# Kernel optimization log

Hardware: AMD Instinct MI355X
Metric: run time of the kernel (lower is better)

Reference implementation:

```python
import jax, jax.numpy as jnp
import numpy as np

ALPHA = 0.2  # leaky relu slope
DEPTH = 3
MAX_REF = 10
MAX_DIR = 32

def leaky(x):
    return jnp.where(x >= 0, x, ALPHA * x)

def setup_inputs() -> dict:
    key = jax.random.key(0)
    ks = jax.random.split(key, 9)
    N, F_IN, F_OUT = 100000, 128, 128
    h = jax.random.normal(ks[0], (N, F_IN), dtype=jnp.float32)
    W_ref = jax.random.normal(ks[1], (F_IN, F_OUT), dtype=jnp.float32) * 0.1
    a_ref = jax.random.normal(ks[2], (2 * F_OUT, 1), dtype=jnp.float32) * 0.1
    W_dir = jax.random.normal(ks[3], (F_IN, F_OUT), dtype=jnp.float32) * 0.1
    a_dir = jax.random.normal(ks[4], (2 * F_OUT, 1), dtype=jnp.float32) * 0.1
    ref_neighbors = jax.random.randint(ks[5], (N, DEPTH + 1, MAX_REF), 0, N)
    ref_counts = jax.random.randint(ks[6], (N, DEPTH + 1), 0, MAX_REF + 1)
    dir_neighbors = jax.random.randint(ks[7], (N, MAX_DIR), 0, N)
    dir_counts = jax.random.randint(ks[8], (N,), 1, MAX_DIR + 1)
    return {"h": h, "W_ref": W_ref, "a_ref": a_ref, "W_dir": W_dir, "a_dir": a_dir,
            "ref_neighbors": ref_neighbors, "ref_counts": ref_counts,
            "dir_neighbors": dir_neighbors, "dir_counts": dir_counts}

def _forward_ref(h, W_ref, a_ref, ref_neighbors, ref_counts):
    Wh = h @ W_ref                                  # [N, F]
    F_ = Wh.shape[1]
    # mean of (up to 10) neighbor features per (node, depth); empty -> zeros
    nbr = Wh[ref_neighbors]                         # [N, D+1, 10, F]
    slot = jnp.arange(MAX_REF)[None, None, :]
    valid = slot < ref_counts[:, :, None]           # [N, D+1, 10]
    cnt = jnp.maximum(ref_counts, 1).astype(Wh.dtype)  # avoid div by 0
    f_ref = jnp.einsum('ndkf,ndk->ndf', nbr, valid.astype(Wh.dtype)) / cnt[:, :, None]  # [N, D+1, F]
    # attention score: leaky(cat(Wh[node], f_ref[d]) @ a_ref)
    a_self, a_nbr = a_ref[:F_, 0], a_ref[F_:, 0]
    e = leaky(Wh @ a_self[:, None] + f_ref @ a_nbr)  # [N,1]+[N,D+1] -> [N, D+1]
    alpha = jax.nn.softmax(e, axis=-1)
    out = jnp.einsum('ndf,nd->nf', f_ref, alpha)
    return jax.nn.sigmoid(out)

def _forward_dir(h, W_dir, a_dir, dir_neighbors, dir_counts):
    Wh = h @ W_dir                                  # [N, F]
    F_ = Wh.shape[1]
    nbr = Wh[dir_neighbors]                         # [N, K, F]
    a_self, a_nbr = a_dir[:F_, 0], a_dir[F_:, 0]
    e = leaky((Wh @ a_self)[:, None] + nbr @ a_nbr)  # [N, K]
    valid = jnp.arange(MAX_DIR)[None, :] < dir_counts[:, None]
    e = jnp.where(valid, e, -jnp.inf)
    alpha = jax.nn.softmax(e, axis=-1)
    out = jnp.einsum('nkf,nk->nf', nbr, alpha)
    return jax.nn.sigmoid(out)

def reference(h, W_ref, a_ref, W_dir, a_dir, ref_neighbors, ref_counts, dir_neighbors, dir_counts):
    h_ref = _forward_ref(h, W_ref, a_ref, ref_neighbors, ref_counts)
    h_dir = _forward_dir(h, W_dir, a_dir, dir_neighbors, dir_counts)
    return (h_ref + h_dir) / 2  # mode='mean'
```

## Files before the change

### kernel.cpp

```cpp
#include <hip/hip_runtime.h>

typedef __attribute__((ext_vector_type(8))) short s16x8;
typedef __attribute__((ext_vector_type(4))) float f32x4;
typedef __attribute__((ext_vector_type(2))) float f32x2;

#define F 128

__device__ __forceinline__ unsigned short f2bf(float f) {
    unsigned int u = __float_as_uint(f);
    u = (u + 0x7fffu + ((u >> 16) & 1u)) >> 16;
    return (unsigned short)u;
}
__device__ __forceinline__ float bflo(unsigned int u) { return __uint_as_float(u << 16); }
__device__ __forceinline__ float bfhi(unsigned int u) { return __uint_as_float(u & 0xffff0000u); }
__device__ __forceinline__ float leaky(float x) { return x >= 0.f ? x : 0.2f * x; }
__device__ __forceinline__ float sigmoidf(float x) { return 1.f / (1.f + __expf(-x)); }

#define SWZ16(row, b) ((b) ^ (((row) & 7) << 4))

__device__ __forceinline__ void glds16(void* lds, const void* g) {
    __builtin_amdgcn_global_load_lds(
        (const __attribute__((address_space(1))) unsigned int*)g,
        (__attribute__((address_space(3))) unsigned int*)lds,
        16, 0, 0);
}

__global__ __launch_bounds__(256) void prep_w(const float* __restrict__ wRef,
                                              const float* __restrict__ wDir,
                                              unsigned short* __restrict__ wT) {
    int i = blockIdx.x * 256 + threadIdx.x;
    int m = i >> 14;
    int rr = i & 16383;
    int k = rr >> 7;
    int c = rr & 127;
    const float* W = m ? wDir : wRef;
    wT[m * 16384 + c * 128 + (k ^ (((c & 7) << 3)))] = f2bf(W[k * 128 + c]);
}

__device__ __forceinline__ void epi(const f32x4* acc, unsigned char* cb ,
                                    int rowBase, int w, int r, int g, int lane, int N,
                                    const float* __restrict__ aVec,
                                    unsigned char* __restrict__ wh ,
                                    float* __restrict__ sArr, float* __restrict__ tArr) {
    float ps[4] = {0.f, 0.f, 0.f, 0.f}, pt[4] = {0.f, 0.f, 0.f, 0.f};
#pragma unroll
    for (int ct = 0; ct < 8; ++ct) {
        int c = ct * 16 + r;
        float As = aVec[c], At = aVec[128 + c];
#pragma unroll
        for (int q = 0; q < 4; ++q) { ps[q] += acc[ct][q] * As; pt[q] += acc[ct][q] * At; }
    }
#pragma unroll
    for (int off = 1; off <= 8; off <<= 1) {
#pragma unroll
        for (int q = 0; q < 4; ++q) {
            ps[q] += __shfl_xor(ps[q], off);
            pt[q] += __shfl_xor(pt[q], off);
        }
    }
    if (r == 0) {
#pragma unroll
        for (int q = 0; q < 4; ++q) {
            int row = rowBase + w * 16 + g * 4 + q;
            if (row < N) { sArr[row] = ps[q]; tArr[row] = pt[q]; }
        }
    }
#pragma unroll
    for (int ct = 0; ct < 8; ++ct) {
#pragma unroll
        for (int q = 0; q < 4; ++q) {
            int lrow = g * 4 + q;
            int xb = (ct * 16 + r) * 2;
            *(unsigned short*)(cb + lrow * 256 + SWZ16(lrow, xb)) = f2bf(acc[ct][q]);
        }
    }
#pragma unroll
    for (int i = 0; i < 4; ++i) {
        int off = i * 1024 + lane * 16;
        int lrow = off >> 8, x = off & 255;
        uint4 v = *(const uint4*)(cb + lrow * 256 + SWZ16(lrow, x));
        int pk0 = __builtin_amdgcn_cvt_pk_fp8_f32(bflo(v.x), bfhi(v.x), 0, false);
        pk0 = __builtin_amdgcn_cvt_pk_fp8_f32(bflo(v.y), bfhi(v.y), pk0, true);
        int pk1 = __builtin_amdgcn_cvt_pk_fp8_f32(bflo(v.z), bfhi(v.z), 0, false);
        pk1 = __builtin_amdgcn_cvt_pk_fp8_f32(bflo(v.w), bfhi(v.w), pk1, true);
        int grow = rowBase + w * 16 + lrow;
        if (grow < N) *(uint2*)(wh + (size_t)grow * 128 + (x >> 1)) = make_uint2((unsigned)pk0, (unsigned)pk1);
    }
}

__global__ __launch_bounds__(256) void gemm_wh(const float* __restrict__ h,
                                               const unsigned short* __restrict__ wT,
                                               const float* __restrict__ aRefG,
                                               const float* __restrict__ aDirG,
                                               unsigned char* __restrict__ whRef,
                                               unsigned char* __restrict__ whDir,
                                               float* __restrict__ sRef, float* __restrict__ tRef,
                                               float* __restrict__ sDir, float* __restrict__ tDir,
                                               int N) {
    __shared__ unsigned char lds[49152];
    const int tid = threadIdx.x;
    const int lane = tid & 63, w = tid >> 6;
    const int r = lane & 15, g = lane >> 4;
    const int rowBase = blockIdx.x * 64;

#pragma unroll
    for (int it = 0; it < 8; ++it) {
        int lin = it * 4096 + tid * 16;
        glds16(lds + 16384 + lin, (const char*)wT + lin);
    }
    float4 av[4][2];
#pragma unroll
    for (int it = 0; it < 4; ++it) {
        int lin = it * 4096 + tid * 16;
        int arow = lin >> 8, x = lin & 255;
        int grow = min(rowBase + arow, N - 1);
        const char* src = (const char*)h + (size_t)grow * 512 + x * 2;
        av[it][0] = *(const float4*)(src);
        av[it][1] = *(const float4*)(src + 16);
    }
#pragma unroll
    for (int it = 0; it < 4; ++it) {
        int lin = it * 4096 + tid * 16;
        int arow = lin >> 8, x = lin & 255;
        s16x8 a;
        a[0] = (short)f2bf(av[it][0].x); a[1] = (short)f2bf(av[it][0].y);
        a[2] = (short)f2bf(av[it][0].z); a[3] = (short)f2bf(av[it][0].w);
        a[4] = (short)f2bf(av[it][1].x); a[5] = (short)f2bf(av[it][1].y);
        a[6] = (short)f2bf(av[it][1].z); a[7] = (short)f2bf(av[it][1].w);
        *(s16x8*)(lds + arow * 256 + SWZ16(arow, x)) = a;
    }
    __syncthreads();

    s16x8 afr[4];
    {
        const int arow = w * 16 + r;
#pragma unroll
        for (int kt = 0; kt < 4; ++kt)
            afr[kt] = *(const s16x8*)(lds + arow * 256 + SWZ16(arow, kt * 64 + g * 16));
    }
    unsigned char* cb = lds + w * 4096;

    {
        f32x4 acc[8];
#pragma unroll
        for (int ct = 0; ct < 8; ++ct) acc[ct] = (f32x4){0.f, 0.f, 0.f, 0.f};
#pragma unroll
        for (int kt = 0; kt < 4; ++kt) {
#pragma unroll
            for (int ct = 0; ct < 8; ++ct) {
                int c = ct * 16 + r;
                s16x8 b = *(const s16x8*)(lds + 16384 + c * 256 + SWZ16(c, kt * 64 + g * 16));
                acc[ct] = __builtin_amdgcn_mfma_f32_16x16x32_bf16(afr[kt], b, acc[ct], 0, 0, 0);
            }
        }
        epi(acc, cb, rowBase, w, r, g, lane, N, aRefG, whRef, sRef, tRef);
    }
    __syncthreads();
#pragma unroll
    for (int it = 0; it < 8; ++it) {
        int lin = it * 4096 + tid * 16;
        glds16(lds + 16384 + lin, (const char*)wT + 32768 + lin);
    }
    __syncthreads();
    {
        f32x4 acc[8];
#pragma unroll
        for (int ct = 0; ct < 8; ++ct) acc[ct] = (f32x4){0.f, 0.f, 0.f, 0.f};
#pragma unroll
        for (int kt = 0; kt < 4; ++kt) {
#pragma unroll
            for (int ct = 0; ct < 8; ++ct) {
                int c = ct * 16 + r;
                s16x8 b = *(const s16x8*)(lds + 16384 + c * 256 + SWZ16(c, kt * 64 + g * 16));
                acc[ct] = __builtin_amdgcn_mfma_f32_16x16x32_bf16(afr[kt], b, acc[ct], 0, 0, 0);
            }
        }
        epi(acc, cb, rowBase, w, r, g, lane, N, aDirG, whDir, sDir, tDir);
    }
}

__device__ __forceinline__ void acc8f8(float* a, uint2 u, float c) {
    f32x2 p0 = __builtin_amdgcn_cvt_pk_f32_fp8((int)u.x, false);
    f32x2 p1 = __builtin_amdgcn_cvt_pk_f32_fp8((int)u.x, true);
    f32x2 p2 = __builtin_amdgcn_cvt_pk_f32_fp8((int)u.y, false);
    f32x2 p3 = __builtin_amdgcn_cvt_pk_f32_fp8((int)u.y, true);
    a[0] += c * p0[0]; a[1] += c * p0[1];
    a[2] += c * p1[0]; a[3] += c * p1[1];
    a[4] += c * p2[0]; a[5] += c * p2[1];
    a[6] += c * p3[0]; a[7] += c * p3[1];
}

__global__ __launch_bounds__(256) void gather_attn(
    const unsigned char* __restrict__ whRef, const unsigned char* __restrict__ whDir,
    const float* __restrict__ sRef, const float* __restrict__ tRef,
    const float* __restrict__ sDir, const float* __restrict__ tDir,
    const int* __restrict__ refNbr, const int* __restrict__ refCnt,
    const int* __restrict__ dirNbr, const int* __restrict__ dirCnt,
    float* __restrict__ out, int N) {
    __shared__ int2 s_list[4][72];

    const int wid = threadIdx.x >> 6;
    const int lane = threadIdx.x & 63;
    const int q = lane >> 4, hl16 = lane & 15;
    const int d = lane >> 4, kk = lane & 15;
    const int n_raw = blockIdx.x * 4 + wid;
    const int n = min(n_raw, N - 1);

    int cnt = refCnt[n * 4 + d];
    bool validR = kk < cnt;
    int idxR = 0;
    float tv = 0.f;
    if (kk < 10) idxR = refNbr[(size_t)n * 40 + d * 10 + kk];
    if (validR) tv = tRef[idxR];
    float sum = tv;
    sum += __shfl_xor(sum, 1); sum += __shfl_xor(sum, 2);
    sum += __shfl_xor(sum, 4); sum += __shfl_xor(sum, 8);
    float rc = 1.f / (float)max(cnt, 1);
    float e = leaky(sRef[n] + sum * rc);
    float mx = fmaxf(e, __shfl_xor(e, 16)); mx = fmaxf(mx, __shfl_xor(mx, 32));
    float wgt = __expf(e - mx);
    float den = wgt + __shfl_xor(wgt, 16); den += __shfl_xor(den, 32);
    float coefR = wgt / den * rc;
    unsigned long long mask = __ballot(validR);
    int pos = (int)__popcll(mask & ((1ull << lane) - 1ull));
    int Lr = (int)__popcll(mask);
    if (validR) s_list[wid][pos] = make_int2(idxR, __float_as_int(coefR));

    int dcnt = dirCnt[n];
    float eD = -1e30f;
    int idxD = 0;
    if (lane < 32) {
        idxD = dirNbr[(size_t)n * 32 + lane];
        if (lane < dcnt) eD = leaky(sDir[n] + tDir[idxD]);
    }
    float mD = eD;
#pragma unroll
    for (int off = 16; off; off >>= 1) mD = fmaxf(mD, __shfl_xor(mD, off, 32));
    float wD = (lane < dcnt) ? __expf(eD - mD) : 0.f;
    float dD = wD;
#pragma unroll
    for (int off = 16; off; off >>= 1) dD += __shfl_xor(dD, off, 32);
    if (lane < dcnt) s_list[wid][40 + lane] = make_int2(idxD, __float_as_int(wD / dD));

    __syncthreads();

    float accR[8] = {0.f, 0.f, 0.f, 0.f, 0.f, 0.f, 0.f, 0.f};
    {
        uint2 u[10]; float c[10];
#pragma unroll
        for (int j = 0; j < 10; ++j) {
            int e = j * 4 + q;
            if (e < Lr) {
                int2 ic = s_list[wid][e];
                c[j] = __int_as_float(ic.y);
                u[j] = *(const uint2*)(whRef + ((size_t)(unsigned)ic.x << 7) + (hl16 << 3));
            }
        }
#pragma unroll
        for (int j = 0; j < 10; ++j) {
            int e = j * 4 + q;
            if (e < Lr) acc8f8(accR, u[j], c[j]);
        }
    }
    float accD[8] = {0.f, 0.f, 0.f, 0.f, 0.f, 0.f, 0.f, 0.f};
    {
        uint2 u[8]; float c[8];
#pragma unroll
        for (int j = 0; j < 8; ++j) {
            int e = j * 4 + q;
            if (e < dcnt) {
                int2 ic = s_list[wid][40 + e];
                c[j] = __int_as_float(ic.y);
                u[j] = *(const uint2*)(whDir + ((size_t)(unsigned)ic.x << 7) + (hl16 << 3));
            }
        }
#pragma unroll
        for (int j = 0; j < 8; ++j) {
            int e = j * 4 + q;
            if (e < dcnt) acc8f8(accD, u[j], c[j]);
        }
    }

#pragma unroll
    for (int j = 0; j < 8; ++j) {
        accR[j] += __shfl_xor(accR[j], 16); accR[j] += __shfl_xor(accR[j], 32);
        accD[j] += __shfl_xor(accD[j], 16); accD[j] += __shfl_xor(accD[j], 32);
    }
    if (n_raw < N && q == 0) {
        float o[8];
#pragma unroll
        for (int j = 0; j < 8; ++j) o[j] = 0.5f * (sigmoidf(accR[j]) + sigmoidf(accD[j]));
        float4* dst = (float4*)(out + (size_t)n * F + hl16 * 8);
        dst[0] = make_float4(o[0], o[1], o[2], o[3]);
        dst[1] = make_float4(o[4], o[5], o[6], o[7]);
    }
}

extern "C" void kernel_launch(void* const* d_in, const int* in_sizes, int n_in,
                              void* d_out, int out_size, void* d_ws, size_t ws_size,
                              hipStream_t stream) {
    const float* h    = (const float*)d_in[0];
    const float* Wref = (const float*)d_in[1];
    const float* aRef = (const float*)d_in[2];
    const float* Wdir = (const float*)d_in[3];
    const float* aDir = (const float*)d_in[4];
    const int* refNbr = (const int*)d_in[5];
    const int* refCnt = (const int*)d_in[6];
    const int* dirNbr = (const int*)d_in[7];
    const int* dirCnt = (const int*)d_in[8];
    float* out = (float*)d_out;
    const int N = in_sizes[0] / F;

    const size_t NF = (size_t)N * F;
    unsigned char* whRef = (unsigned char*)d_ws;
    unsigned char* whDir = whRef + NF;
    float* sRef = (float*)(whDir + NF);
    float* tRef = sRef + N;
    float* sDir = tRef + N;
    float* tDir = sDir + N;
    unsigned short* wT = (unsigned short*)(tDir + N);

    prep_w<<<128, 256, 0, stream>>>(Wref, Wdir, wT);
    gemm_wh<<<(N + 63) / 64, 256, 0, stream>>>(h, wT, aRef, aDir, whRef, whDir,
                                               sRef, tRef, sDir, tDir, N);
    gather_attn<<<(N + 3) / 4, 256, 0, stream>>>(whRef, whDir, sRef, tRef, sDir, tDir,
                                                 refNbr, refCnt, dirNbr, dirCnt, out, N);
}
```

Baseline: 256.2 us.

## Issue neighbor feature gathers before attention softmax and use wave-local LDS fences

Neighbor indices now go into LDS first, so the FP8 feature row gathers for both the ref and dir branches are issued before the attention scores and softmax are computed. Coefficients go into a separate LDS array that is read after the gathers are in flight, which overlaps gather latency with the score and softmax work. The block-wide __syncthreads is replaced by a per-wave lgkmcnt wait plus sched barrier, since each wave only touches its own LDS slice. This keeps 18 uint2 gather results live for longer, which raises register pressure and relies on the waitcnt being enough for cross-lane LDS visibility.

New measurement: 246.0 us. 4.0% less time.

```diff
diff --git a/kernel.cpp b/kernel.cpp
--- a/kernel.cpp
+++ b/kernel.cpp
@@ -17,6 +17,11 @@
 __device__ __forceinline__ float sigmoidf(float x) { return 1.f / (1.f + __expf(-x)); }
 
 #define SWZ16(row, b) ((b) ^ (((row) & 7) << 4))
+
+#define WAVE_LDS_FENCE() do { \
+    asm volatile("s_waitcnt lgkmcnt(0)" ::: "memory"); \
+    __builtin_amdgcn_sched_barrier(0); \
+} while (0)
 
 __device__ __forceinline__ void glds16(void* lds, const void* g) {
     __builtin_amdgcn_global_load_lds(
@@ -197,7 +202,8 @@
     const int* __restrict__ refNbr, const int* __restrict__ refCnt,
     const int* __restrict__ dirNbr, const int* __restrict__ dirCnt,
     float* __restrict__ out, int N) {
-    __shared__ int2 s_list[4][72];
+    __shared__ int   s_idx[4][72];
+    __shared__ float s_coef[4][72];
 
     const int wid = threadIdx.x >> 6;
     const int lane = threadIdx.x & 63;
@@ -207,32 +213,49 @@
     const int n = min(n_raw, N - 1);
 
     int cnt = refCnt[n * 4 + d];
+    int idxR = (kk < 10) ? refNbr[(size_t)n * 40 + d * 10 + kk] : 0;
+    int dcnt = dirCnt[n];
+    int idxD = (lane < 32) ? dirNbr[(size_t)n * 32 + lane] : 0;
+    float sR = sRef[n], sD = sDir[n];
+
     bool validR = kk < cnt;
-    int idxR = 0;
-    float tv = 0.f;
-    if (kk < 10) idxR = refNbr[(size_t)n * 40 + d * 10 + kk];
-    if (validR) tv = tRef[idxR];
+    unsigned long long mask = __ballot(validR);
+    int pos = (int)__popcll(mask & ((1ull << lane) - 1ull));
+    int Lr = (int)__popcll(mask);
+    if (validR) s_idx[wid][pos] = idxR;
+    if (lane < 32) s_idx[wid][40 + lane] = idxD;
+    WAVE_LDS_FENCE();
+
+    uint2 uR[10];
+#pragma unroll
+    for (int j = 0; j < 10; ++j) {
+        int e = j * 4 + q;
+        if (e < Lr)
+            uR[j] = *(const uint2*)(whRef + ((size_t)(unsigned)s_idx[wid][e] << 7) + (hl16 << 3));
+    }
+    uint2 uD[8];
+#pragma unroll
+    for (int j = 0; j < 8; ++j) {
+        int e = j * 4 + q;
+        if (e < dcnt)
+            uD[j] = *(const uint2*)(whDir + ((size_t)(unsigned)s_idx[wid][40 + e] << 7) + (hl16 << 3));
+    }
+
+    float tv = validR ? tRef[idxR] : 0.f;
     float sum = tv;
     sum += __shfl_xor(sum, 1); sum += __shfl_xor(sum, 2);
     sum += __shfl_xor(sum, 4); sum += __shfl_xor(sum, 8);
     float rc = 1.f / (float)max(cnt, 1);
-    float e = leaky(sRef[n] + sum * rc);
+    float e = leaky(sR + sum * rc);
     float mx = fmaxf(e, __shfl_xor(e, 16)); mx = fmaxf(mx, __shfl_xor(mx, 32));
     float wgt = __expf(e - mx);
     float den = wgt + __shfl_xor(wgt, 16); den += __shfl_xor(den, 32);
     float coefR = wgt / den * rc;
-    unsigned long long mask = __ballot(validR);
-    int pos = (int)__popcll(mask & ((1ull << lane) - 1ull));
-    int Lr = (int)__popcll(mask);
-    if (validR) s_list[wid][pos] = make_int2(idxR, __float_as_int(coefR));
-
-    int dcnt = dirCnt[n];
+    if (validR) s_coef[wid][pos] = coefR;
+
     float eD = -1e30f;
-    int idxD = 0;
-    if (lane < 32) {
-        idxD = dirNbr[(size_t)n * 32 + lane];
-        if (lane < dcnt) eD = leaky(sDir[n] + tDir[idxD]);
-    }
+    float tD = (lane < 32 && lane < dcnt) ? tDir[idxD] : 0.f;
+    if (lane < 32 && lane < dcnt) eD = leaky(sD + tD);
     float mD = eD;
 #pragma unroll
     for (int off = 16; off; off >>= 1) mD = fmaxf(mD, __shfl_xor(mD, off, 32));
@@ -240,45 +263,20 @@
     float dD = wD;
 #pragma unroll
     for (int off = 16; off; off >>= 1) dD += __shfl_xor(dD, off, 32);
-    if (lane < dcnt) s_list[wid][40 + lane] = make_int2(idxD, __float_as_int(wD / dD));
-
-    __syncthreads();
+    if (lane < 32 && lane < dcnt) s_coef[wid][40 + lane] = wD / dD;
+    WAVE_LDS_FENCE();
 
     float accR[8] = {0.f, 0.f, 0.f, 0.f, 0.f, 0.f, 0.f, 0.f};
-    {
-        uint2 u[10]; float c[10];
-#pragma unroll
-        for (int j = 0; j < 10; ++j) {
-            int e = j * 4 + q;
-            if (e < Lr) {
-                int2 ic = s_list[wid][e];
-                c[j] = __int_as_float(ic.y);
-                u[j] = *(const uint2*)(whRef + ((size_t)(unsigned)ic.x << 7) + (hl16 << 3));
-            }
-        }
-#pragma unroll
-        for (int j = 0; j < 10; ++j) {
-            int e = j * 4 + q;
-            if (e < Lr) acc8f8(accR, u[j], c[j]);
-        }
+#pragma unroll
+    for (int j = 0; j < 10; ++j) {
+        int e = j * 4 + q;
+        if (e < Lr) acc8f8(accR, uR[j], s_coef[wid][e]);
     }
     float accD[8] = {0.f, 0.f, 0.f, 0.f, 0.f, 0.f, 0.f, 0.f};
-    {
-        uint2 u[8]; float c[8];
-#pragma unroll
-        for (int j = 0; j < 8; ++j) {
-            int e = j * 4 + q;
-            if (e < dcnt) {
-                int2 ic = s_list[wid][40 + e];
-                c[j] = __int_as_float(ic.y);
-                u[j] = *(const uint2*)(whDir + ((size_t)(unsigned)ic.x << 7) + (hl16 << 3));
-            }
-        }
-#pragma unroll
-        for (int j = 0; j < 8; ++j) {
-            int e = j * 4 + q;
-            if (e < dcnt) acc8f8(accD, u[j], c[j]);
-        }
+#pragma unroll
+    for (int j = 0; j < 8; ++j) {
+        int e = j * 4 + q;
+        if (e < dcnt) acc8f8(accD, uD[j], s_coef[wid][40 + e]);
     }
 
 #pragma unroll
```
